# Kernel tuning notes

Measured on AMD Instinct MI355X. Metric: run time of the kernel, lower is better.

The kernel has to match this reference:

```python
import jax, jax.numpy as jnp
import numpy as np

B, L, D, H = 2, 2048, 1024, 16
HD = D // H  # head_dim = 64


def setup_inputs() -> dict:
    key = jax.random.key(0)
    ks = jax.random.split(key, 5)
    x = jax.random.normal(ks[0], (B, L, D), dtype=jnp.float32)
    # causal mask: True means masked (as in masked_fill)
    mask = jnp.triu(jnp.ones((L, L), dtype=bool), k=1)[None, None, :, :]
    W_qkv = jax.random.normal(ks[1], (3 * D, D), dtype=jnp.float32) * (1.0 / np.sqrt(D))
    b_qkv = jax.random.normal(ks[2], (3 * D,), dtype=jnp.float32) * 0.02
    W_out = jax.random.normal(ks[3], (D, D), dtype=jnp.float32) * (1.0 / np.sqrt(D))
    b_out = jax.random.normal(ks[4], (D,), dtype=jnp.float32) * 0.02
    return {"x": x, "mask": mask, "W_qkv": W_qkv, "b_qkv": b_qkv,
            "W_out": W_out, "b_out": b_out}


def reference(x, mask, W_qkv, b_qkv, W_out, b_out):
    b, l, d = x.shape
    qkv = x @ W_qkv.T + b_qkv                       # (b, l, 3d)
    q, k, v = jnp.split(qkv, 3, axis=-1)
    # (b, l, d) -> (b, h, l, hd)
    to_heads = lambda t: t.reshape(b, l, H, HD).transpose(0, 2, 1, 3)
    q, k, v = to_heads(q), to_heads(k), to_heads(v)
    scale = 1.0 / jnp.sqrt(jnp.float32(HD))
    a = jnp.einsum('bhqd,bhkd->bhqk', q, k) * scale  # (b, h, l, l)
    a = jnp.where(mask, -jnp.inf, a)
    a = jax.nn.softmax(a, axis=-1)
    out = jnp.einsum('bhqk,bhkd->bhqd', a, v)        # (b, h, l, hd)
    out = out.transpose(0, 2, 1, 3).reshape(b, l, d)
    out = out @ W_out.T + b_out
    return out
```

## Files before the change

### kernel.cpp

```cpp
#include <hip/hip_runtime.h>
#include <hip/hip_bf16.h>

#define LOG2E 1.44269504088896340736f

typedef __attribute__((ext_vector_type(8))) short short8_t;
typedef __attribute__((ext_vector_type(4))) float f32x4_t;
typedef __attribute__((ext_vector_type(4))) unsigned short us4_t;

__device__ __forceinline__ unsigned short f2bf(float f) {
  unsigned u = __builtin_bit_cast(unsigned, f);
  return (unsigned short)((u + 0x7fffu + ((u >> 16) & 1u)) >> 16);
}

__device__ __forceinline__ void gload_lds16(const unsigned short* g, unsigned short* l) {
  __builtin_amdgcn_global_load_lds(
      (const __attribute__((address_space(1))) void*)(g),
      (__attribute__((address_space(3))) void*)(l), 16, 0, 0);
}

__global__ __launch_bounds__(256) void cvt3(
    const float* __restrict__ x, const float* __restrict__ wq, const float* __restrict__ wo,
    unsigned short* __restrict__ xb, unsigned short* __restrict__ wqb,
    unsigned short* __restrict__ wob)
{
  const int n1 = 4096 * 1024 / 4, n2 = 3072 * 1024 / 4, n3 = 1024 * 1024 / 4;
  const int total = n1 + n2 + n3;
  for (int t = blockIdx.x * blockDim.x + threadIdx.x; t < total; t += gridDim.x * blockDim.x) {
    const float* s; unsigned short* d; int off;
    if (t < n1)            { s = x;  d = xb;  off = t * 4; }
    else if (t < n1 + n2)  { s = wq; d = wqb; off = (t - n1) * 4; }
    else                   { s = wo; d = wob; off = (t - n1 - n2) * 4; }
    f32x4_t v = *(const f32x4_t*)(s + off);
    us4_t o = { f2bf(v[0]), f2bf(v[1]), f2bf(v[2]), f2bf(v[3]) };
    *(us4_t*)(d + off) = o;
  }
}

template<int MODE>
__global__ __launch_bounds__(256) void gemm_bt(
    const unsigned short* __restrict__ A, const unsigned short* __restrict__ Bw,
    const float* __restrict__ bias, float* __restrict__ Cf,
    unsigned short* __restrict__ Qp, unsigned short* __restrict__ Kp,
    unsigned short* __restrict__ Vtp, int M, int N, int K)
{
  __shared__ alignas(16) unsigned short lA[128 * 32];
  __shared__ alignas(16) unsigned short lB[128 * 32];
  const int tid = threadIdx.x, lane = tid & 63, w = tid >> 6;
  const int lo = lane & 15, hi = lane >> 4;
  const int bm = blockIdx.y * 128, bn = blockIdx.x * 128;
  const int wm = (w >> 1) * 64, wn = (w & 1) * 64;

  const f32x4_t zero = {0.f, 0.f, 0.f, 0.f};
  f32x4_t acc[4][4];
#pragma unroll
  for (int i = 0; i < 4; ++i)
#pragma unroll
    for (int j = 0; j < 4; ++j) acc[i][j] = zero;

  const unsigned short* gA[2]; const unsigned short* gB[2];
  unsigned short* lAp[2]; unsigned short* lBp[2];
#pragma unroll
  for (int i = 0; i < 2; ++i) {
    int offb = (i * 4 + w) * 1024;
    int off  = offb + lane * 16;
    int row  = off >> 6;
    int ke   = (off & 63) >> 1;
    gA[i]  = &A [(size_t)(bm + row) * K + ke];
    gB[i]  = &Bw[(size_t)(bn + row) * K + ke];
    lAp[i] = &lA[offb >> 1];
    lBp[i] = &lB[offb >> 1];
  }

  for (int k0 = 0; k0 < K; k0 += 32) {
#pragma unroll
    for (int i = 0; i < 2; ++i) {
      gload_lds16(gA[i] + k0, lAp[i]);
      gload_lds16(gB[i] + k0, lBp[i]);
    }
    __syncthreads();
    short8_t af[4], bb[4];
#pragma unroll
    for (int i = 0; i < 4; ++i) af[i] = *(const short8_t*)&lA[(wm + i * 16 + lo) * 32 + hi * 8];
#pragma unroll
    for (int j = 0; j < 4; ++j) bb[j] = *(const short8_t*)&lB[(wn + j * 16 + lo) * 32 + hi * 8];
#pragma unroll
    for (int i = 0; i < 4; ++i)
#pragma unroll
      for (int j = 0; j < 4; ++j)
        acc[i][j] = __builtin_amdgcn_mfma_f32_16x16x32_bf16(af[i], bb[j], acc[i][j], 0, 0, 0);
    __syncthreads();
  }

#pragma unroll
  for (int i = 0; i < 4; ++i) {
#pragma unroll
    for (int j = 0; j < 4; ++j) {
      int col = bn + wn + j * 16 + lo;
      float bv = bias[col];
#pragma unroll
      for (int r = 0; r < 4; ++r) {
        int row = bm + wm + i * 16 + hi * 4 + r;
        float v = acc[i][j][r] + bv;
        if (MODE == 1) {
          Cf[(size_t)row * N + col] = v;
        } else {
          unsigned short hv = f2bf(v);
          int sec = col >> 10, h = (col >> 6) & 15, d = col & 63;
          int b = row >> 11, ll = row & 2047;
          int bh = b * 16 + h;
          if (sec == 0)      Qp [((size_t)bh * 2048 + ll) * 64 + d] = hv;
          else if (sec == 1) Kp [((size_t)bh * 2048 + ll) * 64 + d] = hv;
          else               Vtp[((size_t)bh * 64 + d) * 2048 + ll] = hv;
        }
      }
    }
  }
}

__global__ __launch_bounds__(256) void attn(
    const unsigned short* __restrict__ Q, const unsigned short* __restrict__ K,
    const unsigned short* __restrict__ V, unsigned short* __restrict__ AO)
{
  const int tid = threadIdx.x, lane = tid & 63, w = tid >> 6;
  const int lo = lane & 15, hi = lane >> 4;
  const int qt = 31 - blockIdx.y;
  const int bh = blockIdx.x;
  const int qbase = qt * 64 + w * 16;
  const int nt = qt + 1;
  const unsigned short* Qb = Q + (size_t)bh * 2048 * 64;
  const unsigned short* Kb = K + (size_t)bh * 2048 * 64;
  const unsigned short* Vb = V + (size_t)bh * 64 * 2048;

  __shared__ alignas(16) unsigned short lK[2][8 * 512];
  __shared__ alignas(16) unsigned short lV[2][8 * 512];
  __shared__ alignas(16) unsigned short pl[4][16 * 72];
  unsigned short* myP = &pl[w][0];

  short8_t qf0 = *(const short8_t*)&Qb[(qbase + lo) * 64 + hi * 8];
  short8_t qf1 = *(const short8_t*)&Qb[(qbase + lo) * 64 + 32 + hi * 8];

  const f32x4_t zero = {0.f, 0.f, 0.f, 0.f};
  f32x4_t o[4] = {zero, zero, zero, zero};
  float m[4] = {-INFINITY, -INFINITY, -INFINITY, -INFINITY};
  float l[4] = {0.f, 0.f, 0.f, 0.f};
  const float SC = 0.125f * LOG2E;
  const float THR = 8.0f;

  const unsigned short* ksrc = Kb + (size_t)lane * 64 + 2 * w * 8;
  const unsigned short* vsrc = Vb + (size_t)lane * 2048 + 2 * w * 8;
  unsigned short* kd0 = &lK[0][2 * w * 512];
  unsigned short* kd1 = &lK[1][2 * w * 512];
  unsigned short* vd0 = &lV[0][2 * w * 512];
  unsigned short* vd1 = &lV[1][2 * w * 512];

  gload_lds16(ksrc,     kd0);
  gload_lds16(ksrc + 8, kd0 + 512);
  gload_lds16(vsrc,     vd0);
  gload_lds16(vsrc + 8, vd0 + 512);

  for (int t = 0; t < nt; ++t) {
    const int kb = t * 64;
    const int cur = t & 1;
    __syncthreads();

    if (t + 1 < nt) {
      const unsigned short* ks = ksrc + (size_t)(kb + 64) * 64;
      const unsigned short* vs = vsrc + (kb + 64);
      unsigned short* kd = cur ? kd0 : kd1;
      unsigned short* vd = cur ? vd0 : vd1;
      gload_lds16(ks,     kd);
      gload_lds16(ks + 8, kd + 512);
      gload_lds16(vs,     vd);
      gload_lds16(vs + 8, vd + 512);
    }
    const unsigned short* lk = cur ? &lK[1][0] : &lK[0][0];
    const unsigned short* lv = cur ? &lV[1][0] : &lV[0][0];

    f32x4_t s4[4] = {zero, zero, zero, zero};
    __builtin_amdgcn_s_setprio(1);
#pragma unroll
    for (int s = 0; s < 4; ++s) {
      short8_t k0 = *(const short8_t*)&lk[(hi * 64 + s * 16 + lo) * 8];
      short8_t k1 = *(const short8_t*)&lk[((4 + hi) * 64 + s * 16 + lo) * 8];
      s4[s] = __builtin_amdgcn_mfma_f32_16x16x32_bf16(qf0, k0, s4[s], 0, 0, 0);
      s4[s] = __builtin_amdgcn_mfma_f32_16x16x32_bf16(qf1, k1, s4[s], 0, 0, 0);
    }
    __builtin_amdgcn_s_setprio(0);

    const bool needmask = (kb + 64 > qbase);
    float a[4][4];
    float pm[4];
#pragma unroll
    for (int r = 0; r < 4; ++r) {
      int q = qbase + hi * 4 + r;
#pragma unroll
      for (int s = 0; s < 4; ++s) {
        float av = s4[s][r] * SC;
        if (needmask && (kb + s * 16 + lo > q)) av = -INFINITY;
        a[r][s] = av;
      }
      pm[r] = fmaxf(fmaxf(a[r][0], a[r][1]), fmaxf(a[r][2], a[r][3]));
    }

    bool ok = (pm[0] - m[0] <= THR) && (pm[1] - m[1] <= THR) &&
              (pm[2] - m[2] <= THR) && (pm[3] - m[3] <= THR);
    if (!__all(ok)) {
#pragma unroll
      for (int r = 0; r < 4; ++r) {
        float t2 = pm[r];
        t2 = fmaxf(t2, __shfl_xor(t2, 1));
        t2 = fmaxf(t2, __shfl_xor(t2, 2));
        t2 = fmaxf(t2, __shfl_xor(t2, 4));
        t2 = fmaxf(t2, __shfl_xor(t2, 8));
        float mn = fmaxf(m[r], t2);
        float f = __builtin_amdgcn_exp2f(m[r] - mn);
        m[r] = mn;
        l[r] *= f;
#pragma unroll
        for (int j = 0; j < 4; ++j) o[j][r] *= f;
      }
    }

#pragma unroll
    for (int r = 0; r < 4; ++r) {
      float e0 = __builtin_amdgcn_exp2f(a[r][0] - m[r]);
      float e1 = __builtin_amdgcn_exp2f(a[r][1] - m[r]);
      float e2 = __builtin_amdgcn_exp2f(a[r][2] - m[r]);
      float e3 = __builtin_amdgcn_exp2f(a[r][3] - m[r]);
      l[r] += (e0 + e1) + (e2 + e3);
      int prow = (hi * 4 + r) * 72;
      myP[prow + lo]      = f2bf(e0);
      myP[prow + 16 + lo] = f2bf(e1);
      myP[prow + 32 + lo] = f2bf(e2);
      myP[prow + 48 + lo] = f2bf(e3);
    }

    short8_t pf0 = *(const short8_t*)&myP[lo * 72 + hi * 8];
    short8_t pf1 = *(const short8_t*)&myP[lo * 72 + 32 + hi * 8];
    __builtin_amdgcn_s_setprio(1);
#pragma unroll
    for (int j = 0; j < 4; ++j) {
      short8_t v0 = *(const short8_t*)&lv[(hi * 64 + j * 16 + lo) * 8];
      short8_t v1 = *(const short8_t*)&lv[((4 + hi) * 64 + j * 16 + lo) * 8];
      o[j] = __builtin_amdgcn_mfma_f32_16x16x32_bf16(pf0, v0, o[j], 0, 0, 0);
      o[j] = __builtin_amdgcn_mfma_f32_16x16x32_bf16(pf1, v1, o[j], 0, 0, 0);
    }
    __builtin_amdgcn_s_setprio(0);
  }

  const int b = bh >> 4, h = bh & 15;
#pragma unroll
  for (int r = 0; r < 4; ++r) {
    float ls = l[r];
    ls += __shfl_xor(ls, 1);
    ls += __shfl_xor(ls, 2);
    ls += __shfl_xor(ls, 4);
    ls += __shfl_xor(ls, 8);
    float inv = 1.0f / ls;
    int qrow = qbase + hi * 4 + r;
    size_t base = ((size_t)b * 2048 + qrow) * 1024 + h * 64;
#pragma unroll
    for (int j = 0; j < 4; ++j)
      AO[base + j * 16 + lo] = f2bf(o[j][r] * inv);
  }
}

extern "C" void kernel_launch(void* const* d_in, const int* in_sizes, int n_in,
                              void* d_out, int out_size, void* d_ws, size_t ws_size,
                              hipStream_t stream)
{
  (void)in_sizes; (void)n_in; (void)out_size; (void)ws_size;
  const float* x    = (const float*)d_in[0];
  const float* Wqkv = (const float*)d_in[2];
  const float* bqkv = (const float*)d_in[3];
  const float* Wout = (const float*)d_in[4];
  const float* bout = (const float*)d_in[5];

  unsigned short* ws  = (unsigned short*)d_ws;
  unsigned short* xb  = ws;
  unsigned short* wqb = xb  + 4096 * 1024;
  unsigned short* wob = wqb + 3072 * 1024;
  unsigned short* Qp  = wob + 1024 * 1024;
  unsigned short* Kp  = Qp  + 32 * 2048 * 64;
  unsigned short* Vtp = Kp  + 32 * 2048 * 64;
  unsigned short* AO  = Vtp + 32 * 2048 * 64;

  cvt3<<<dim3(2048), dim3(256), 0, stream>>>(x, Wqkv, Wout, xb, wqb, wob);
  gemm_bt<0><<<dim3(24, 32), dim3(256), 0, stream>>>(
      xb, wqb, bqkv, nullptr, Qp, Kp, Vtp, 4096, 3072, 1024);
  attn<<<dim3(32, 32), dim3(256), 0, stream>>>(Qp, Kp, Vtp, AO);
  gemm_bt<1><<<dim3(8, 32), dim3(256), 0, stream>>>(
      AO, wob, bout, (float*)d_out, nullptr, nullptr, nullptr, 4096, 1024, 1024);
}
```

Before: 231.0 us.

## Swizzle GEMM block order, pad k-major LDS layout, shrink out-proj tile

Both GEMMs now run on a 1-D grid whose block index is remapped by an XCD-aware swizzle (lid&7 times a stride), so neighbouring tiles land on the same chiplet and share L2. The LDS tiles are reorganised into k-chunk-major panels padded to 1040/528 elements to avoid bank conflicts on the fragment reads. The output-projection GEMM uses a 128x64 tile, giving 512 blocks instead of 256 and better CU coverage on the smaller N=1024 problem. The cost is more complex index math and lower per-block reuse in the second GEMM.

```diff
diff --git a/kernel.cpp b/kernel.cpp
--- a/kernel.cpp
+++ b/kernel.cpp
@@ -43,48 +43,76 @@
     unsigned short* __restrict__ Qp, unsigned short* __restrict__ Kp,
     unsigned short* __restrict__ Vtp, int M, int N, int K)
 {
-  __shared__ alignas(16) unsigned short lA[128 * 32];
-  __shared__ alignas(16) unsigned short lB[128 * 32];
+  constexpr int BN   = (MODE == 0) ? 128 : 64;
+  constexpr int NT_N = (MODE == 0) ? 24 : 16;
+  constexpr int CPX  = (MODE == 0) ? 96 : 64;
+  constexpr int ACK  = 1040;
+  constexpr int BCK  = (MODE == 0) ? 1040 : 528;
+
+  __shared__ alignas(16) unsigned short lAl[4 * ACK];
+  __shared__ alignas(16) unsigned short lBl[4 * BCK];
+
   const int tid = threadIdx.x, lane = tid & 63, w = tid >> 6;
   const int lo = lane & 15, hi = lane >> 4;
-  const int bm = blockIdx.y * 128, bn = blockIdx.x * 128;
-  const int wm = (w >> 1) * 64, wn = (w & 1) * 64;
+
+  const int lid = blockIdx.x;
+  const int swz = (lid & 7) * CPX + (lid >> 3);
+  const int bm = (swz / NT_N) * 128;
+  const int bn = (swz % NT_N) * BN;
 
   const f32x4_t zero = {0.f, 0.f, 0.f, 0.f};
-  f32x4_t acc[4][4];
-#pragma unroll
-  for (int i = 0; i < 4; ++i)
+  constexpr int MI = (MODE == 0) ? 4 : 2;
+  f32x4_t acc[MI][4];
+#pragma unroll
+  for (int i = 0; i < MI; ++i)
 #pragma unroll
     for (int j = 0; j < 4; ++j) acc[i][j] = zero;
 
-  const unsigned short* gA[2]; const unsigned short* gB[2];
-  unsigned short* lAp[2]; unsigned short* lBp[2];
+  const unsigned short* gA[2]; unsigned short* lAp[2];
 #pragma unroll
   for (int i = 0; i < 2; ++i) {
-    int offb = (i * 4 + w) * 1024;
-    int off  = offb + lane * 16;
-    int row  = off >> 6;
-    int ke   = (off & 63) >> 1;
-    gA[i]  = &A [(size_t)(bm + row) * K + ke];
-    gB[i]  = &Bw[(size_t)(bn + row) * K + ke];
-    lAp[i] = &lA[offb >> 1];
-    lBp[i] = &lB[offb >> 1];
-  }
+    int s  = (i * 4 + w) * 64;
+    int sl = s + lane;
+    gA[i]  = &A[(size_t)(bm + (sl & 127)) * K + (sl >> 7) * 8];
+    lAp[i] = &lAl[(s >> 7) * ACK + (s & 127) * 8];
+  }
+  const unsigned short* gB[2]; unsigned short* lBp[2];
+  if (MODE == 0) {
+#pragma unroll
+    for (int i = 0; i < 2; ++i) {
+      int s  = (i * 4 + w) * 64;
+      int sl = s + lane;
+      gB[i]  = &Bw[(size_t)(bn + (sl & 127)) * K + (sl >> 7) * 8];
+      lBp[i] = &lBl[(s >> 7) * BCK + (s & 127) * 8];
+    }
+  } else {
+    gB[0]  = &Bw[(size_t)(bn + lane) * K + w * 8];
+    lBp[0] = &lBl[w * BCK];
+    gB[1]  = nullptr; lBp[1] = nullptr;
+  }
+
+  const int wm = (MODE == 0) ? (w >> 1) * 64 : w * 32;
+  const int wn = (MODE == 0) ? (w & 1) * 64 : 0;
 
   for (int k0 = 0; k0 < K; k0 += 32) {
 #pragma unroll
-    for (int i = 0; i < 2; ++i) {
-      gload_lds16(gA[i] + k0, lAp[i]);
-      gload_lds16(gB[i] + k0, lBp[i]);
+    for (int i = 0; i < 2; ++i) gload_lds16(gA[i] + k0, lAp[i]);
+    if (MODE == 0) {
+#pragma unroll
+      for (int i = 0; i < 2; ++i) gload_lds16(gB[i] + k0, lBp[i]);
+    } else {
+      gload_lds16(gB[0] + k0, lBp[0]);
     }
     __syncthreads();
-    short8_t af[4], bb[4];
-#pragma unroll
-    for (int i = 0; i < 4; ++i) af[i] = *(const short8_t*)&lA[(wm + i * 16 + lo) * 32 + hi * 8];
-#pragma unroll
-    for (int j = 0; j < 4; ++j) bb[j] = *(const short8_t*)&lB[(wn + j * 16 + lo) * 32 + hi * 8];
-#pragma unroll
-    for (int i = 0; i < 4; ++i)
+    short8_t af[MI], bb[4];
+#pragma unroll
+    for (int i = 0; i < MI; ++i)
+      af[i] = *(const short8_t*)&lAl[hi * ACK + (wm + i * 16 + lo) * 8];
+#pragma unroll
+    for (int j = 0; j < 4; ++j)
+      bb[j] = *(const short8_t*)&lBl[hi * BCK + (wn + j * 16 + lo) * 8];
+#pragma unroll
+    for (int i = 0; i < MI; ++i)
 #pragma unroll
       for (int j = 0; j < 4; ++j)
         acc[i][j] = __builtin_amdgcn_mfma_f32_16x16x32_bf16(af[i], bb[j], acc[i][j], 0, 0, 0);
@@ -92,7 +120,7 @@
   }
 
 #pragma unroll
-  for (int i = 0; i < 4; ++i) {
+  for (int i = 0; i < MI; ++i) {
 #pragma unroll
     for (int j = 0; j < 4; ++j) {
       int col = bn + wn + j * 16 + lo;
@@ -286,9 +314,9 @@
   unsigned short* AO  = Vtp + 32 * 2048 * 64;
 
   cvt3<<<dim3(2048), dim3(256), 0, stream>>>(x, Wqkv, Wout, xb, wqb, wob);
-  gemm_bt<0><<<dim3(24, 32), dim3(256), 0, stream>>>(
+  gemm_bt<0><<<dim3(768), dim3(256), 0, stream>>>(
       xb, wqb, bqkv, nullptr, Qp, Kp, Vtp, 4096, 3072, 1024);
   attn<<<dim3(32, 32), dim3(256), 0, stream>>>(Qp, Kp, Vtp, AO);
-  gemm_bt<1><<<dim3(8, 32), dim3(256), 0, stream>>>(
+  gemm_bt<1><<<dim3(512), dim3(256), 0, stream>>>(
       AO, wob, bout, (float*)d_out, nullptr, nullptr, nullptr, 4096, 1024, 1024);
 }
```

Result: slower. 247.9 us (+7.3%).
